# Performance work log

Hardware: AMD Instinct MI355X
Metric: run time of the kernel (lower is better)

## Reference

```python
import jax, jax.numpy as jnp
import numpy as np

OBS, ACT, EMB, HID, NQ = 512, 32, 512, 512, 32
B = 32768


def setup_inputs() -> dict:
    key = jax.random.key(0)
    ks = jax.random.split(key, 12)
    s_in = 1.0 / np.sqrt(OBS + ACT)
    s_emb = 1.0 / np.sqrt(EMB)
    s_hid = 1.0 / np.sqrt(HID)
    return {
        "observation": jax.random.normal(ks[0], (B, OBS), jnp.float32),
        "prev_action": jax.random.normal(ks[1], (B, ACT), jnp.float32),
        "hidden_state": jax.random.normal(ks[2], (HID,), jnp.float32),
        "cell_state": jax.random.normal(ks[3], (HID,), jnp.float32),
        "W1": jax.random.uniform(ks[4], (EMB, OBS + ACT), jnp.float32, -s_in, s_in),
        "b1": jax.random.uniform(ks[5], (EMB,), jnp.float32, -s_in, s_in),
        "W_ih": jax.random.uniform(ks[6], (4 * HID, EMB), jnp.float32, -s_hid, s_hid),
        "b_ih": jax.random.uniform(ks[7], (4 * HID,), jnp.float32, -s_hid, s_hid),
        "W_hh": jax.random.uniform(ks[8], (4 * HID, HID), jnp.float32, -s_hid, s_hid),
        "b_hh": jax.random.uniform(ks[9], (4 * HID,), jnp.float32, -s_hid, s_hid),
        "W2": jax.random.uniform(ks[10], (NQ, HID), jnp.float32, -s_hid, s_hid),
        "b2": jax.random.uniform(ks[11], (NQ,), jnp.float32, -s_hid, s_hid),
    }


def reference(observation, prev_action, hidden_state, cell_state,
              W1, b1, W_ih, b_ih, W_hh, b_hh, W2, b2):
    # MLP1: Linear + ReLU over concat(obs, prev_action)  -> [B, EMB]
    x = jnp.concatenate([observation, prev_action], axis=-1)
    x = jax.nn.relu(x @ W1.T + b1)

    # Original torch code loops LSTMCell over batch, but reuses the SAME
    # (hidden_state, cell_state) every iteration -> fully batchable.
    # gates: [B, 4H]; h contribution is identical for all rows (broadcast).
    gates = x @ W_ih.T + b_ih + (hidden_state @ W_hh.T + b_hh)
    i, f, g, o = jnp.split(gates, 4, axis=-1)  # torch LSTMCell gate order
    i = jax.nn.sigmoid(i)
    f = jax.nn.sigmoid(f)
    g = jnp.tanh(g)
    o = jax.nn.sigmoid(o)
    c_new = f * cell_state + i * g          # [B, HID]
    h_new = o * jnp.tanh(c_new)             # [B, HID]

    q_values = h_new @ W2.T + b2             # [B, NQ]
    # torch returns last loop iteration's (h, c)
    return q_values, h_new[-1], c_new[-1]
```

## Files before the change

### kernel.cpp

```cpp
#include <hip/hip_runtime.h>
#include <stdint.h>

#define DEVINL __device__ __forceinline__

typedef __attribute__((ext_vector_type(8))) __bf16 bf16x8;
typedef __attribute__((ext_vector_type(4))) float f32x4;
typedef __attribute__((ext_vector_type(2))) long longx2;

DEVINL unsigned short f2bf(float f) {
  union { float f; unsigned int u; } v; v.f = f;
  unsigned int u = v.u;
  return (unsigned short)((u + 0x7fffu + ((u >> 16) & 1u)) >> 16);
}

DEVINL unsigned char f2fp8(float f) {
  return (unsigned char)(__builtin_amdgcn_cvt_pk_fp8_f32(f, f, 0, false) & 0xff);
}

DEVINL float sigm(float x) { return __builtin_amdgcn_rcpf(1.f + __expf(-x)); }
DEVINL float tanh_(float x) {
  return 1.f - 2.f * __builtin_amdgcn_rcpf(1.f + __expf(2.f * x));
}

DEVINL int pcol(int gn) {
  return (gn & ~63) | ((((gn & 31) >> 3)) << 4) | (((gn >> 5) & 1) << 3) | (gn & 7);
}

#define GLD_LDS16(gptr, lptr)                                                  \
  __builtin_amdgcn_global_load_lds(                                            \
      (__attribute__((address_space(1))) void*)(gptr),                         \
      (__attribute__((address_space(3))) void*)(lptr), 16, 0, 0)

#define TOPBAR_4 asm volatile("s_waitcnt vmcnt(4) lgkmcnt(0)\n\ts_barrier" ::: "memory")
#define TOPBAR_1 asm volatile("s_waitcnt vmcnt(1) lgkmcnt(0)\n\ts_barrier" ::: "memory")
#define TOPBAR_0 asm volatile("s_waitcnt vmcnt(0) lgkmcnt(0)\n\ts_barrier" ::: "memory")
#define BOTBAR   asm volatile("s_waitcnt lgkmcnt(0)\n\ts_barrier" ::: "memory")

DEVINL int swz_col(int c) { return ((c & 3) ^ ((c >> 3) & 3)) * 8; }
DEVINL int swz16(int c) { return ((c & 3) ^ ((c >> 3) & 3)) * 16; }

__global__ void prep_all(const float* __restrict__ obs, const float* __restrict__ act,
                         const float* __restrict__ W1, const float* __restrict__ Wih,
                         const float* __restrict__ W2, const float* __restrict__ Whh,
                         const float* __restrict__ hid, const float* __restrict__ bhh,
                         const float* __restrict__ bih,
                         unsigned short* __restrict__ A0, unsigned short* __restrict__ W1b,
                         unsigned char* __restrict__ Wih8, unsigned short* __restrict__ W2b,
                         float* __restrict__ hvec) {
  const int bid = blockIdx.x, tid = threadIdx.x;
  if (bid < 2176) {
    const int total = 32768 * 68;
    for (int c = bid * 256 + tid; c < total; c += 2176 * 256) {
      const int b = c / 68, c8 = c % 68;
      const float* src = (c8 < 64) ? (obs + (size_t)b * 512 + c8 * 8)
                                   : (act + (size_t)b * 32 + (c8 - 64) * 8);
      float4 f0 = *(const float4*)src;
      float4 f1 = *(const float4*)(src + 4);
      unsigned short u[8] = {f2bf(f0.x), f2bf(f0.y), f2bf(f0.z), f2bf(f0.w),
                             f2bf(f1.x), f2bf(f1.y), f2bf(f1.z), f2bf(f1.w)};
      *(uint4*)(A0 + (size_t)b * 544 + c8 * 8) = *(uint4*)u;
    }
  } else if (bid < 2176 + 1312) {
    const int i = (bid - 2176) * 256 + tid;
    if (i < 69632) {
      float4 f = *(const float4*)(W1 + (size_t)i * 4);
      unsigned short u[4] = {f2bf(f.x), f2bf(f.y), f2bf(f.z), f2bf(f.w)};
      *(uint2*)(W1b + (size_t)i * 4) = *(uint2*)u;
    } else if (i < 69632 + 262144) {
      const int off = i - 69632;
      const int row = off >> 7, col0 = (off & 127) * 4;
      float4 f = *(const float4*)(Wih + (size_t)off * 4);
      int pk = __builtin_amdgcn_cvt_pk_fp8_f32(f.x * 16.f, f.y * 16.f, 0, false);
      pk = __builtin_amdgcn_cvt_pk_fp8_f32(f.z * 16.f, f.w * 16.f, pk, true);
      *(unsigned int*)(Wih8 + (size_t)row * 512 + pcol(col0)) = (unsigned int)pk;
    } else {
      const int off = i - 331776;
      float4 f = *(const float4*)(W2 + (size_t)off * 4);
      unsigned short u[4] = {f2bf(f.x), f2bf(f.y), f2bf(f.z), f2bf(f.w)};
      *(uint2*)(W2b + (size_t)off * 4) = *(uint2*)u;
    }
  } else {
    const int j = (bid - 3488) * 4 + (tid >> 6);
    const int lane = tid & 63;
    const float* w = Whh + (size_t)j * 512;
    float s = 0.f;
    for (int k = lane; k < 512; k += 64) s += w[k] * hid[k];
    for (int off = 32; off; off >>= 1) s += __shfl_down(s, off, 64);
    if (lane == 0) hvec[j] = s + bhh[j] + bih[j];
  }
}

__global__ __launch_bounds__(256, 2) void gemm1_relu(
    const unsigned short* __restrict__ A0,
    const unsigned short* __restrict__ W1b,
    const float* __restrict__ b1,
    unsigned char* __restrict__ X8) {
  constexpr int KT = 17, LD = 544;
  __shared__ __align__(16) unsigned short As[2][128 * 32];
  __shared__ __align__(16) unsigned short Bs[2][128 * 32];
  const int tid = threadIdx.x, wave = tid >> 6, lane = tid & 63;
  const int id = blockIdx.x, xcd = id & 7, slot = id >> 3;
  const int m0 = (xcd * 32 + (slot >> 2)) * 128;
  const int n0 = (slot & 3) * 128;
  const int wr = (wave >> 1) * 64, wc = (wave & 1) * 64;
  f32x4 acc[4][4] = {};

  const int c0 = tid, c1 = tid + 256;
  const unsigned short* pA0 = A0 + (size_t)(m0 + (c0 >> 2)) * LD + swz_col(c0);
  const unsigned short* pA1 = A0 + (size_t)(m0 + (c1 >> 2)) * LD + swz_col(c1);
  const unsigned short* pB0 = W1b + (size_t)(n0 + (c0 >> 2)) * LD + swz_col(c0);
  const unsigned short* pB1 = W1b + (size_t)(n0 + (c1 >> 2)) * LD + swz_col(c1);
  const int fr = lane & 15, q = lane >> 4;
  const int koff = (q ^ ((fr >> 1) & 3)) * 8;

#define STAGE1(buf)                                                            \
  do {                                                                         \
    GLD_LDS16(pA0, &As[(buf)][wave * 512]);                                    \
    GLD_LDS16(pA1, &As[(buf)][2048 + wave * 512]);                             \
    GLD_LDS16(pB0, &Bs[(buf)][wave * 512]);                                    \
    GLD_LDS16(pB1, &Bs[(buf)][2048 + wave * 512]);                             \
    pA0 += 32; pA1 += 32; pB0 += 32; pB1 += 32;                                \
  } while (0)

  STAGE1(0);
  for (int kt = 0; kt < KT; ++kt) {
    if (kt + 1 < KT) { STAGE1((kt + 1) & 1); TOPBAR_4; } else { TOPBAR_0; }
    const unsigned short* as = As[kt & 1];
    const unsigned short* bs = Bs[kt & 1];
    bf16x8 a[4], b[4];
#pragma unroll
    for (int i = 0; i < 4; ++i) a[i] = *(const bf16x8*)&as[(wr + i * 16 + fr) * 32 + koff];
#pragma unroll
    for (int j = 0; j < 4; ++j) b[j] = *(const bf16x8*)&bs[(wc + j * 16 + fr) * 32 + koff];
#pragma unroll
    for (int i = 0; i < 4; ++i)
#pragma unroll
      for (int j = 0; j < 4; ++j)
        acc[i][j] = __builtin_amdgcn_mfma_f32_16x16x32_bf16(a[i], b[j], acc[i][j], 0, 0, 0);
    BOTBAR;
  }
#undef STAGE1
  const int rbase = q * 4, cn = fr;
#pragma unroll
  for (int i = 0; i < 4; ++i)
#pragma unroll
    for (int j = 0; j < 4; ++j) {
      const int gn = n0 + wc + j * 16 + cn;
      const int pc = pcol(gn);
      const float bias = b1[gn];
#pragma unroll
      for (int r = 0; r < 4; ++r) {
        const int gm = m0 + wr + i * 16 + rbase + r;
        float v = acc[i][j][r] + bias;
        v = v > 0.f ? v : 0.f;
        X8[(size_t)gm * 512 + pc] = f2fp8(v * 8.f);
      }
    }
}

__global__ __launch_bounds__(256, 4) void gemm2_lstm(
    const unsigned char* __restrict__ X8,
    const unsigned char* __restrict__ Wih8,
    const float* __restrict__ hvec,
    const float* __restrict__ cell,
    unsigned short* __restrict__ H,
    float* __restrict__ hlast,
    float* __restrict__ clast) {
  constexpr int KT = 8;
  __shared__ __align__(16) unsigned char As[2][128 * 64];
  __shared__ __align__(16) unsigned char Bs[2][4 * 32 * 64];
  const int tid = threadIdx.x, wave = tid >> 6, lane = tid & 63;
  const int id = blockIdx.x, xcd = id & 7, slot = id >> 3;
  const int m0 = (xcd * 32 + (slot >> 4)) * 128;
  const int n0 = (slot & 15) * 32;
  const int wr = (wave >> 1) * 64, wc = (wave & 1) * 16;
  f32x4 acc[4][4] = {};

  const int c0 = tid, c1 = tid + 256;
  const unsigned char* pA0 = X8 + (size_t)(m0 + (c0 >> 2)) * 512 + swz16(c0);
  const unsigned char* pA1 = X8 + (size_t)(m0 + (c1 >> 2)) * 512 + swz16(c1);
  const unsigned char* pB0 =
      Wih8 + (size_t)((c0 >> 7) * 512 + n0 + ((c0 >> 2) & 31)) * 512 + swz16(c0);
  const unsigned char* pB1 =
      Wih8 + (size_t)((c1 >> 7) * 512 + n0 + ((c1 >> 2) & 31)) * 512 + swz16(c1);
  const int fr = lane & 15, q = lane >> 4;
  const int koff = (q ^ ((fr >> 1) & 3)) * 16;

#define STAGE2(buf)                                                            \
  do {                                                                         \
    GLD_LDS16(pA0, &As[(buf)][wave * 1024]);                                   \
    GLD_LDS16(pA1, &As[(buf)][4096 + wave * 1024]);                            \
    GLD_LDS16(pB0, &Bs[(buf)][wave * 1024]);                                   \
    GLD_LDS16(pB1, &Bs[(buf)][4096 + wave * 1024]);                            \
    pA0 += 64; pA1 += 64; pB0 += 64; pB1 += 64;                                \
  } while (0)

  STAGE2(0);
  for (int kt = 0; kt < KT; ++kt) {
    if (kt + 1 < KT) { STAGE2((kt + 1) & 1); TOPBAR_4; } else { TOPBAR_0; }
    const unsigned char* as = As[kt & 1];
    const unsigned char* bs = Bs[kt & 1];
    longx2 a[4], b[4];
#pragma unroll
    for (int i = 0; i < 4; ++i)
      a[i] = *(const longx2*)&as[(wr + i * 16 + fr) * 64 + koff];
#pragma unroll
    for (int qd = 0; qd < 4; ++qd)
      b[qd] = *(const longx2*)&bs[qd * 2048 + (wc + fr) * 64 + koff];
#pragma unroll
    for (int i = 0; i < 4; ++i)
#pragma unroll
      for (int qd = 0; qd < 4; ++qd) {
        acc[i][qd] =
            __builtin_amdgcn_mfma_f32_16x16x32_fp8_fp8(a[i].x, b[qd].x, acc[i][qd], 0, 0, 0);
        acc[i][qd] =
            __builtin_amdgcn_mfma_f32_16x16x32_fp8_fp8(a[i].y, b[qd].y, acc[i][qd], 0, 0, 0);
      }
    BOTBAR;
  }
#undef STAGE2
  const int rbase = q * 4, cn = fr;
  const int gn = n0 + wc + cn;
  const float hv_i = hvec[gn];
  const float hv_f = hvec[gn + 512];
  const float hv_g = hvec[gn + 1024];
  const float hv_o = hvec[gn + 1536];
  const float cprev = cell[gn];
  constexpr float S = 1.f / 128.f;
#pragma unroll
  for (int i = 0; i < 4; ++i)
#pragma unroll
    for (int r = 0; r < 4; ++r) {
      const int gm = m0 + wr + i * 16 + rbase + r;
      float si = sigm(acc[i][0][r] * S + hv_i);
      float sf = sigm(acc[i][1][r] * S + hv_f);
      float tg = tanh_(acc[i][2][r] * S + hv_g);
      float so = sigm(acc[i][3][r] * S + hv_o);
      float cnew = sf * cprev + si * tg;
      float hnew = so * tanh_(cnew);
      H[(size_t)gm * 512 + gn] = f2bf(hnew);
      if (gm == 32767) { hlast[gn] = hnew; clast[gn] = cnew; }
    }
}

__global__ __launch_bounds__(256, 2) void gemm3(
    const unsigned short* __restrict__ H,
    const unsigned short* __restrict__ W2b,
    const float* __restrict__ b2,
    float* __restrict__ Q) {
  constexpr int KT = 16, LDW = 520;
  __shared__ __align__(16) unsigned short As[2][64 * 32];
  __shared__ __align__(16) unsigned short Ws[32 * LDW];
  const int tid = threadIdx.x, wave = tid >> 6, lane = tid & 63;
  const int id = blockIdx.x;
  const int m0 = ((id & 7) * 64 + (id >> 3)) * 64;
  for (int c = tid; c < 2048; c += 256) {
    const int row = c >> 6, col8 = c & 63;
    *(uint4*)&Ws[row * LDW + col8 * 8] = *(const uint4*)(W2b + row * 512 + col8 * 8);
  }
  f32x4 acc[2] = {};
  const int c0 = tid;
  const unsigned short* pA0 = H + (size_t)(m0 + (c0 >> 2)) * 512 + swz_col(c0);
  const int fr = lane & 15, q = lane >> 4;
  const int koff = (q ^ ((fr >> 1) & 3)) * 8;

#define STAGE3(buf)                                                            \
  do {                                                                         \
    GLD_LDS16(pA0, &As[(buf)][wave * 512]);                                    \
    pA0 += 32;                                                                 \
  } while (0)

  STAGE3(0);
  for (int kt = 0; kt < KT; ++kt) {
    if (kt + 1 < KT) { STAGE3((kt + 1) & 1); TOPBAR_1; } else { TOPBAR_0; }
    const unsigned short* as = As[kt & 1];
    const int k0 = kt * 32;
    bf16x8 a  = *(const bf16x8*)&as[(wave * 16 + fr) * 32 + koff];
    bf16x8 b0 = *(const bf16x8*)&Ws[fr * LDW + k0 + q * 8];
    bf16x8 b1 = *(const bf16x8*)&Ws[(16 + fr) * LDW + k0 + q * 8];
    acc[0] = __builtin_amdgcn_mfma_f32_16x16x32_bf16(a, b0, acc[0], 0, 0, 0);
    acc[1] = __builtin_amdgcn_mfma_f32_16x16x32_bf16(a, b1, acc[1], 0, 0, 0);
    BOTBAR;
  }
#undef STAGE3
  const int rbase = q * 4;
#pragma unroll
  for (int j = 0; j < 2; ++j) {
    const int gn = j * 16 + fr;
    const float bias = b2[gn];
#pragma unroll
    for (int r = 0; r < 4; ++r) {
      const int gm = m0 + wave * 16 + rbase + r;
      Q[(size_t)gm * 32 + gn] = acc[j][r] + bias;
    }
  }
}

extern "C" void kernel_launch(void* const* d_in, const int* in_sizes, int n_in,
                              void* d_out, int out_size, void* d_ws, size_t ws_size,
                              hipStream_t stream) {
  const float* obs  = (const float*)d_in[0];
  const float* act  = (const float*)d_in[1];
  const float* hid  = (const float*)d_in[2];
  const float* cell = (const float*)d_in[3];
  const float* W1   = (const float*)d_in[4];
  const float* b1   = (const float*)d_in[5];
  const float* Wih  = (const float*)d_in[6];
  const float* bih  = (const float*)d_in[7];
  const float* Whh  = (const float*)d_in[8];
  const float* bhh  = (const float*)d_in[9];
  const float* W2   = (const float*)d_in[10];
  const float* b2   = (const float*)d_in[11];
  float* out = (float*)d_out;

  char* ws = (char*)d_ws;
  unsigned short* A0   = (unsigned short*)(ws);
  unsigned short* H    = (unsigned short*)(ws);
  unsigned char*  X8   = (unsigned char*)(ws + 35651584);
  unsigned short* W1b  = (unsigned short*)(ws + 52428800);
  unsigned char*  Wih8 = (unsigned char*)(ws + 52985856);
  unsigned short* W2b  = (unsigned short*)(ws + 54034432);
  float*          hvec = (float*)(ws + 54067200);

  prep_all<<<4000, 256, 0, stream>>>(obs, act, W1, Wih, W2, Whh, hid, bhh, bih,
                                     A0, W1b, Wih8, W2b, hvec);
  gemm1_relu<<<1024, 256, 0, stream>>>(A0, W1b, b1, X8);
  gemm2_lstm<<<4096, 256, 0, stream>>>(X8, Wih8, hvec, cell, H,
                                       out + 32768 * 32,
                                       out + 32768 * 32 + 512);
  gemm3<<<512, 256, 0, stream>>>(H, W2b, b2, out);
}
```

Measured before the change: 213.3 us.

## Fuse output projection into LSTM GEMM via split-K atomic accumulation

The final W2 projection is folded into the LSTM gate kernel. Each block stages its 128x32 slice of h in LDS as bf16 and multiplies it by the matching 32-column slice of W2 with MFMA. The partial Q sums are accumulated into the output with float atomicAdd, and the prep kernel pre-fills Q with the bias. This removes writing and re-reading the 32MB bf16 H buffer and one kernel launch. In exchange it adds 16-way atomic contention per Q element and makes the summation order nondeterministic.

Result: no change. 216.3 us (+1.4%).

```diff
diff --git a/kernel.cpp b/kernel.cpp
--- a/kernel.cpp
+++ b/kernel.cpp
@@ -43,10 +43,10 @@
                          const float* __restrict__ W1, const float* __restrict__ Wih,
                          const float* __restrict__ W2, const float* __restrict__ Whh,
                          const float* __restrict__ hid, const float* __restrict__ bhh,
-                         const float* __restrict__ bih,
+                         const float* __restrict__ bih, const float* __restrict__ b2,
                          unsigned short* __restrict__ A0, unsigned short* __restrict__ W1b,
                          unsigned char* __restrict__ Wih8, unsigned short* __restrict__ W2b,
-                         float* __restrict__ hvec) {
+                         float* __restrict__ hvec, float* __restrict__ qout) {
   const int bid = blockIdx.x, tid = threadIdx.x;
   if (bid < 2176) {
     const int total = 32768 * 68;
@@ -79,7 +79,7 @@
       unsigned short u[4] = {f2bf(f.x), f2bf(f.y), f2bf(f.z), f2bf(f.w)};
       *(uint2*)(W2b + (size_t)off * 4) = *(uint2*)u;
     }
-  } else {
+  } else if (bid < 2176 + 1312 + 512) {
     const int j = (bid - 3488) * 4 + (tid >> 6);
     const int lane = tid & 63;
     const float* w = Whh + (size_t)j * 512;
@@ -87,6 +87,11 @@
     for (int k = lane; k < 512; k += 64) s += w[k] * hid[k];
     for (int off = 32; off; off >>= 1) s += __shfl_down(s, off, 64);
     if (lane == 0) hvec[j] = s + bhh[j] + bih[j];
+  } else {
+    const int c = (bid - 4000) * 256 + tid;
+    const int row = c >> 3, j4 = c & 7;
+    float4 b = *(const float4*)(b2 + j4 * 4);
+    *(float4*)(qout + (size_t)row * 32 + j4 * 4) = b;
   }
 }
 
@@ -158,17 +163,21 @@
     }
 }
 
-__global__ __launch_bounds__(256, 4) void gemm2_lstm(
+__global__ __launch_bounds__(256, 4) void gemm23_lstm(
     const unsigned char* __restrict__ X8,
     const unsigned char* __restrict__ Wih8,
+    const unsigned short* __restrict__ W2b,
     const float* __restrict__ hvec,
     const float* __restrict__ cell,
-    unsigned short* __restrict__ H,
+    float* __restrict__ qout,
     float* __restrict__ hlast,
     float* __restrict__ clast) {
   constexpr int KT = 8;
-  __shared__ __align__(16) unsigned char As[2][128 * 64];
-  __shared__ __align__(16) unsigned char Bs[2][4 * 32 * 64];
+  __shared__ __align__(16) unsigned char LDSB[4 * 8192];
+#define AS2(buf) (LDSB + (buf) * 8192)
+#define BS2(buf) (LDSB + 16384 + (buf) * 8192)
+  unsigned short* hs = (unsigned short*)LDSB;
+  constexpr int LDH = 40;
   const int tid = threadIdx.x, wave = tid >> 6, lane = tid & 63;
   const int id = blockIdx.x, xcd = id & 7, slot = id >> 3;
   const int m0 = (xcd * 32 + (slot >> 4)) * 128;
@@ -188,18 +197,18 @@
 
 #define STAGE2(buf)                                                            \
   do {                                                                         \
-    GLD_LDS16(pA0, &As[(buf)][wave * 1024]);                                   \
-    GLD_LDS16(pA1, &As[(buf)][4096 + wave * 1024]);                            \
-    GLD_LDS16(pB0, &Bs[(buf)][wave * 1024]);                                   \
-    GLD_LDS16(pB1, &Bs[(buf)][4096 + wave * 1024]);                            \
+    GLD_LDS16(pA0, AS2(buf) + wave * 1024);                                    \
+    GLD_LDS16(pA1, AS2(buf) + 4096 + wave * 1024);                             \
+    GLD_LDS16(pB0, BS2(buf) + wave * 1024);                                    \
+    GLD_LDS16(pB1, BS2(buf) + 4096 + wave * 1024);                             \
     pA0 += 64; pA1 += 64; pB0 += 64; pB1 += 64;                                \
   } while (0)
 
   STAGE2(0);
   for (int kt = 0; kt < KT; ++kt) {
     if (kt + 1 < KT) { STAGE2((kt + 1) & 1); TOPBAR_4; } else { TOPBAR_0; }
-    const unsigned char* as = As[kt & 1];
-    const unsigned char* bs = Bs[kt & 1];
+    const unsigned char* as = AS2(kt & 1);
+    const unsigned char* bs = BS2(kt & 1);
     longx2 a[4], b[4];
 #pragma unroll
     for (int i = 0; i < 4; ++i)
@@ -219,6 +228,7 @@
     BOTBAR;
   }
 #undef STAGE2
+
   const int rbase = q * 4, cn = fr;
   const int gn = n0 + wc + cn;
   const float hv_i = hvec[gn];
@@ -231,69 +241,43 @@
   for (int i = 0; i < 4; ++i)
 #pragma unroll
     for (int r = 0; r < 4; ++r) {
-      const int gm = m0 + wr + i * 16 + rbase + r;
+      const int rl = wr + i * 16 + rbase + r;
       float si = sigm(acc[i][0][r] * S + hv_i);
       float sf = sigm(acc[i][1][r] * S + hv_f);
       float tg = tanh_(acc[i][2][r] * S + hv_g);
       float so = sigm(acc[i][3][r] * S + hv_o);
       float cnew = sf * cprev + si * tg;
       float hnew = so * tanh_(cnew);
-      H[(size_t)gm * 512 + gn] = f2bf(hnew);
-      if (gm == 32767) { hlast[gn] = hnew; clast[gn] = cnew; }
-    }
-}
-
-__global__ __launch_bounds__(256, 2) void gemm3(
-    const unsigned short* __restrict__ H,
-    const unsigned short* __restrict__ W2b,
-    const float* __restrict__ b2,
-    float* __restrict__ Q) {
-  constexpr int KT = 16, LDW = 520;
-  __shared__ __align__(16) unsigned short As[2][64 * 32];
-  __shared__ __align__(16) unsigned short Ws[32 * LDW];
-  const int tid = threadIdx.x, wave = tid >> 6, lane = tid & 63;
-  const int id = blockIdx.x;
-  const int m0 = ((id & 7) * 64 + (id >> 3)) * 64;
-  for (int c = tid; c < 2048; c += 256) {
-    const int row = c >> 6, col8 = c & 63;
-    *(uint4*)&Ws[row * LDW + col8 * 8] = *(const uint4*)(W2b + row * 512 + col8 * 8);
+      hs[rl * LDH + (wc + cn)] = f2bf(hnew);
+      if (m0 + rl == 32767) { hlast[gn] = hnew; clast[gn] = cnew; }
+    }
+  BOTBAR;
+
+  f32x4 qacc[2][2] = {};
+  bf16x8 wfrag[2];
+#pragma unroll
+  for (int jt = 0; jt < 2; ++jt)
+    wfrag[jt] = *(const bf16x8*)(W2b + (size_t)(jt * 16 + fr) * 512 + n0 + q * 8);
+#pragma unroll
+  for (int i2 = 0; i2 < 2; ++i2) {
+    bf16x8 afrag = *(const bf16x8*)&hs[(wave * 32 + i2 * 16 + fr) * LDH + q * 8];
+#pragma unroll
+    for (int jt = 0; jt < 2; ++jt)
+      qacc[i2][jt] = __builtin_amdgcn_mfma_f32_16x16x32_bf16(afrag, wfrag[jt], qacc[i2][jt], 0, 0, 0);
   }
-  f32x4 acc[2] = {};
-  const int c0 = tid;
-  const unsigned short* pA0 = H + (size_t)(m0 + (c0 >> 2)) * 512 + swz_col(c0);
-  const int fr = lane & 15, q = lane >> 4;
-  const int koff = (q ^ ((fr >> 1) & 3)) * 8;
-
-#define STAGE3(buf)                                                            \
-  do {                                                                         \
-    GLD_LDS16(pA0, &As[(buf)][wave * 512]);                                    \
-    pA0 += 32;                                                                 \
-  } while (0)
-
-  STAGE3(0);
-  for (int kt = 0; kt < KT; ++kt) {
-    if (kt + 1 < KT) { STAGE3((kt + 1) & 1); TOPBAR_1; } else { TOPBAR_0; }
-    const unsigned short* as = As[kt & 1];
-    const int k0 = kt * 32;
-    bf16x8 a  = *(const bf16x8*)&as[(wave * 16 + fr) * 32 + koff];
-    bf16x8 b0 = *(const bf16x8*)&Ws[fr * LDW + k0 + q * 8];
-    bf16x8 b1 = *(const bf16x8*)&Ws[(16 + fr) * LDW + k0 + q * 8];
-    acc[0] = __builtin_amdgcn_mfma_f32_16x16x32_bf16(a, b0, acc[0], 0, 0, 0);
-    acc[1] = __builtin_amdgcn_mfma_f32_16x16x32_bf16(a, b1, acc[1], 0, 0, 0);
-    BOTBAR;
-  }
-#undef STAGE3
-  const int rbase = q * 4;
-#pragma unroll
-  for (int j = 0; j < 2; ++j) {
-    const int gn = j * 16 + fr;
-    const float bias = b2[gn];
-#pragma unroll
-    for (int r = 0; r < 4; ++r) {
-      const int gm = m0 + wave * 16 + rbase + r;
-      Q[(size_t)gm * 32 + gn] = acc[j][r] + bias;
-    }
-  }
+#pragma unroll
+  for (int i2 = 0; i2 < 2; ++i2)
+#pragma unroll
+    for (int jt = 0; jt < 2; ++jt) {
+      const int col = jt * 16 + fr;
+#pragma unroll
+      for (int r = 0; r < 4; ++r) {
+        const int row = m0 + wave * 32 + i2 * 16 + q * 4 + r;
+        atomicAdd(&qout[(size_t)row * 32 + col], qacc[i2][jt][r]);
+      }
+    }
+#undef AS2
+#undef BS2
 }
 
 extern "C" void kernel_launch(void* const* d_in, const int* in_sizes, int n_in,
@@ -315,18 +299,16 @@
 
   char* ws = (char*)d_ws;
   unsigned short* A0   = (unsigned short*)(ws);
-  unsigned short* H    = (unsigned short*)(ws);
   unsigned char*  X8   = (unsigned char*)(ws + 35651584);
   unsigned short* W1b  = (unsigned short*)(ws + 52428800);
   unsigned char*  Wih8 = (unsigned char*)(ws + 52985856);
   unsigned short* W2b  = (unsigned short*)(ws + 54034432);
   float*          hvec = (float*)(ws + 54067200);
 
-  prep_all<<<4000, 256, 0, stream>>>(obs, act, W1, Wih, W2, Whh, hid, bhh, bih,
-                                     A0, W1b, Wih8, W2b, hvec);
+  prep_all<<<5024, 256, 0, stream>>>(obs, act, W1, Wih, W2, Whh, hid, bhh, bih, b2,
+                                     A0, W1b, Wih8, W2b, hvec, out);
   gemm1_relu<<<1024, 256, 0, stream>>>(A0, W1b, b1, X8);
-  gemm2_lstm<<<4096, 256, 0, stream>>>(X8, Wih8, hvec, cell, H,
-                                       out + 32768 * 32,
-                                       out + 32768 * 32 + 512);
-  gemm3<<<512, 256, 0, stream>>>(H, W2b, b2, out);
-}
+  gemm23_lstm<<<4096, 256, 0, stream>>>(X8, Wih8, W2b, hvec, cell, out,
+                                        out + 32768 * 32,
+                                        out + 32768 * 32 + 512);
+}
```
